# Kernel optimization log

Measured on AMD Instinct MI355X. Metric: run time of the kernel, lower is better.

## Reference

```python
import jax, jax.numpy as jnp
import numpy as np

THRESH = 0.5
DECAY = 0.2

B = 16384
IN_DIM = 784
HID = 400
OUT = 10


def act_fun(mem):
    # spike = (mem > thresh).float()
    return (mem > THRESH).astype(mem.dtype)


def setup_inputs() -> dict:
    key = jax.random.key(0)
    kx, k1, k2, k3, k4 = jax.random.split(key, 5)
    x = jax.random.uniform(kx, (B, IN_DIM), dtype=jnp.float32)  # pixel probs in [0,1]
    W1 = jax.random.normal(k1, (HID, IN_DIM), dtype=jnp.float32) * (1.0 / np.sqrt(IN_DIM))
    b1 = jax.random.normal(k2, (HID,), dtype=jnp.float32) * 0.01
    W2 = jax.random.normal(k3, (OUT, HID), dtype=jnp.float32) * (1.0 / np.sqrt(HID))
    b2 = jax.random.normal(k4, (OUT,), dtype=jnp.float32) * 0.01
    return {"x": x, "W1": W1, "b1": b1, "W2": W2, "b2": b2, "time_window": 20}


def reference(x, W1, b1, W2, b2, time_window):
    Bsz = x.shape[0]
    keys = jax.random.split(jax.random.key(42), time_window)

    def step(carry, k):
        h1_mem, h1_spike, h2_mem, h2_spike, h2_sum = carry
        u = jax.random.uniform(k, x.shape, dtype=x.dtype)
        xi = (x > u).astype(x.dtype)  # Bernoulli spike encoding of input
        # LIF layer 1
        h1_mem = h1_mem * DECAY * (1.0 - h1_spike) + xi @ W1.T + b1
        h1_spike = act_fun(h1_mem)
        # LIF layer 2
        h2_mem = h2_mem * DECAY * (1.0 - h2_spike) + h1_spike @ W2.T + b2
        h2_spike = act_fun(h2_mem)
        return (h1_mem, h1_spike, h2_mem, h2_spike, h2_sum + h2_spike), None

    z_h = jnp.zeros((Bsz, HID), dtype=x.dtype)
    z_o = jnp.zeros((Bsz, OUT), dtype=x.dtype)
    init = (z_h, z_h, z_o, z_o, z_o)
    (_, _, _, _, h2_sum), _ = jax.lax.scan(step, init, keys)
    return h2_sum / time_window
```

## Files before the change

### kernel.cpp

```cpp
#include <hip/hip_runtime.h>
#include <stdint.h>


#define INDIM  784
#define HID    400
#define ODIM   10
#define TSTEPS 20
#define NS     16384

#define KW     25
#define NCOL   416
#define NB_N   13
#define BROWG  202
#define BROWL  203
#define MS     256
#define NLIMB  5

#define XI_DW   ((size_t)TSTEPS * NS * KW)
#define SPK_OFF (XI_DW)
#define SPK_DW  ((size_t)NS * TSTEPS * NB_N)
#define BL_OFF  (XI_DW + SPK_DW)
#define WS_NEED ((XI_DW + SPK_DW + (size_t)NLIMB * NCOL * BROWG) * 4)

#define TD   8
#define NT   98
#define WTJ  512
#define XIW  26
#define SPW  14

typedef int i32x4  __attribute__((ext_vector_type(4)));
typedef int i32x16 __attribute__((ext_vector_type(16)));

__device__ __forceinline__ void tfr(uint32_t& x0, uint32_t& x1, int r) {
  x0 += x1;
  x1 = (x1 << r) | (x1 >> (32 - r));
  x1 ^= x0;
}

__device__ __forceinline__ uint2 tf2x32(uint32_t k0, uint32_t k1,
                                        uint32_t c0, uint32_t c1) {
  uint32_t k2 = k0 ^ k1 ^ 0x1BD11BDAu;
  uint32_t x0 = c0 + k0, x1 = c1 + k1;
  tfr(x0,x1,13); tfr(x0,x1,15); tfr(x0,x1,26); tfr(x0,x1,6);
  x0 += k1; x1 += k2 + 1u;
  tfr(x0,x1,17); tfr(x0,x1,29); tfr(x0,x1,16); tfr(x0,x1,24);
  x0 += k2; x1 += k0 + 2u;
  tfr(x0,x1,13); tfr(x0,x1,15); tfr(x0,x1,26); tfr(x0,x1,6);
  x0 += k0; x1 += k1 + 3u;
  tfr(x0,x1,17); tfr(x0,x1,29); tfr(x0,x1,16); tfr(x0,x1,24);
  x0 += k1; x1 += k2 + 4u;
  tfr(x0,x1,13); tfr(x0,x1,15); tfr(x0,x1,26); tfr(x0,x1,6);
  x0 += k2; x1 += k0 + 5u;
  return make_uint2(x0, x1);
}

__device__ __forceinline__ float bits_to_unif(uint32_t b) {
  return __uint_as_float((b >> 9) | 0x3f800000u) - 1.0f;
}


__global__ __launch_bounds__(256, 4)
void snn_prep(const float* __restrict__ x, const float* __restrict__ W1,
              uint32_t* __restrict__ ws) {
  const int tid = threadIdx.x, bid = blockIdx.x;
  if (bid < 4096) {
    const int wv = tid >> 6, lane = tid & 63;
    const int s  = bid * 4 + wv;
    float xv[13];
#pragma unroll
    for (int c = 0; c < 13; ++c) {
      const int d = c * 64 + lane;
      xv[c] = (d < INDIM) ? x[s * INDIM + d] : 0.0f;
    }
    for (int t = 0; t < TSTEPS; ++t) {
      const uint2 kt = tf2x32(0u, 42u, 0u, (uint32_t)t);
      uint32_t* dst = ws + ((size_t)t * NS + s) * KW;
#pragma unroll
      for (int c = 0; c < 13; ++c) {
        const int d = c * 64 + lane;
        int xb = 0;
        if (d < INDIM) {
          uint2 r = tf2x32(kt.x, kt.y, 0u, (uint32_t)(s * INDIM + d));
          xb = xv[c] > bits_to_unif(r.x ^ r.y);
        }
        unsigned long long m = __ballot(xb);
        if (lane == 0) {
          dst[2*c] = (uint32_t)m;
          if (2*c + 1 < KW) dst[2*c + 1] = (uint32_t)(m >> 32);
        }
      }
    }
  } else {
    const int idx = (bid - 4096) * 256 + tid;
    if (idx < NCOL * BROWG) {
      const int col = idx / BROWG, grp = idx - col * BROWG;
      uint32_t dw[NLIMB] = {0u, 0u, 0u, 0u, 0u};
#pragma unroll
      for (int b = 0; b < 4; ++b) {
        const int d = grp * 4 + b;
        double w = 0.0;
        if (col < HID && d < INDIM) w = (double)W1[col * INDIM + d];
        long long V = (long long)rint(w * 0x1p41);
        const long long CAP = 547599908735ll;
        if (V >  CAP) V =  CAP;
        if (V < -CAP) V = -CAP;
#pragma unroll
        for (int l = 0; l < NLIMB; ++l) {
          const int r = (int)(((V + 128) & 255) - 128);
          dw[l] |= ((uint32_t)(uint8_t)(int8_t)r) << (8 * b);
          V = (V - r) >> 8;
        }
      }
      uint32_t* bl = ws + BL_OFF;
#pragma unroll
      for (int l = 0; l < NLIMB; ++l)
        bl[((size_t)l * NCOL + col) * BROWG + grp] = dw[l];
    }
  }
}

__global__ __launch_bounds__(256, 2)
void snn_l1(const float* __restrict__ b1, uint32_t* __restrict__ ws) {
  __shared__ uint32_t xi_lds[MS * KW];
  __shared__ uint32_t blds[2][32 * BROWL];

  const int tid  = threadIdx.x;
  const int nb   = blockIdx.x % NB_N;
  const int mb   = blockIdx.x / NB_N;
  const int n0   = nb * 32, sbase = mb * MS;
  const int wv   = tid >> 6, lane = tid & 63;
  const int half = lane >> 5, c31 = lane & 31;
  const int col  = n0 + c31;
  const double bb = (col < HID) ? (double)b1[col] : 0.0;

  const uint32_t* xi_ws  = ws;
  uint32_t*       spk_ws = ws + SPK_OFF;
  const uint32_t* bl_ws  = ws + BL_OFF;

  auto stageB = [&](int l, int buf) {
    if (tid < BROWG) {
      const uint32_t* src = bl_ws + ((size_t)l * NCOL + n0) * BROWG + tid;
      uint32_t* dst = &blds[buf][tid];
#pragma unroll
      for (int c = 0; c < 32; ++c)
        dst[c * BROWL] = src[c * BROWG];
    }
  };
  auto stageXi = [&](int t) {
    const uint32_t* src = xi_ws + ((size_t)t * NS + sbase) * KW;
#pragma unroll
    for (int j = 0; j < KW; ++j)
      xi_lds[tid + j * 256] = src[tid + j * 256];
  };

  double mem[2][16];
  uint32_t sp[2] = {0u, 0u};
#pragma unroll
  for (int T = 0; T < 2; ++T)
#pragma unroll
    for (int i = 0; i < 16; ++i) mem[T][i] = 0.0;

  stageB(0, 0);
  stageXi(0);
  __syncthreads();

  int cur = 0;
  for (int t = 0; t < TSTEPS; ++t) {
#pragma unroll
    for (int T = 0; T < 2; ++T)
#pragma unroll
      for (int i = 0; i < 16; ++i)
        mem[T][i] = ((sp[T] >> i) & 1u) ? 0.0 : mem[T][i] * 0.2;

    double sc = 0x1p-41;
    for (int l = 0; l < NLIMB; ++l) {
      stageB((l + 1) % NLIMB, cur ^ 1);

      i32x16 acc0, acc1;
#pragma unroll
      for (int i = 0; i < 16; ++i) { acc0[i] = 0; acc1[i] = 0; }

      const uint32_t* xr0 = &xi_lds[(wv * 64 +  0 + c31) * KW];
      const uint32_t* xr1 = &xi_lds[(wv * 64 + 32 + c31) * KW];
      const uint32_t* bp0 = &blds[cur][c31 * BROWL + half * 4];

#pragma unroll 5
      for (int ks = 0; ks < 25; ++ks) {
        const uint32_t hw0 = (xr0[ks] >> (16 * half)) & 0xFFFFu;
        const uint32_t hw1 = (xr1[ks] >> (16 * half)) & 0xFFFFu;
        i32x4 a0, a1, bfr;
#pragma unroll
        for (int q = 0; q < 4; ++q) {
          a0[q] = (int)((((hw0 >> (4*q)) & 0xFu) * 0x00204081u) & 0x01010101u);
          a1[q] = (int)((((hw1 >> (4*q)) & 0xFu) * 0x00204081u) & 0x01010101u);
        }
        const uint32_t* bp = bp0 + ks * 8;
        const uint2 p0 = *(const uint2*)(bp);
        const uint2 p1 = *(const uint2*)(bp + 2);
        bfr[0] = (int)p0.x; bfr[1] = (int)p0.y;
        bfr[2] = (int)p1.x; bfr[3] = (int)p1.y;
        acc0 = __builtin_amdgcn_mfma_i32_32x32x32_i8(a0, bfr, acc0, 0, 0, 0);
        acc1 = __builtin_amdgcn_mfma_i32_32x32x32_i8(a1, bfr, acc1, 0, 0, 0);
      }

#pragma unroll
      for (int i = 0; i < 16; ++i) {
        mem[0][i] += (double)acc0[i] * sc;
        mem[1][i] += (double)acc1[i] * sc;
      }
      sc *= 256.0;
      __syncthreads();
      cur ^= 1;
    }

    uint32_t m0 = 0u, m1 = 0u;
#pragma unroll
    for (int i = 0; i < 16; ++i) {
      mem[0][i] += bb;  if (mem[0][i] > 0.5) m0 |= (1u << i);
      mem[1][i] += bb;  if (mem[1][i] > 0.5) m1 |= (1u << i);
    }
    sp[0] = m0; sp[1] = m1;

#pragma unroll
    for (int T = 0; T < 2; ++T) {
      const uint32_t mm = T ? m1 : m0;
#pragma unroll
      for (int rg = 0; rg < 16; ++rg) {
        unsigned long long bm = __ballot((mm >> rg) & 1u);
        if (lane == 0) {
          const int rlo  = (rg & 3) + 8 * (rg >> 2);
          const int srow = sbase + wv * 64 + T * 32 + rlo;
          spk_ws[((size_t)srow * TSTEPS + t) * NB_N + nb] = (uint32_t)bm;
          spk_ws[((size_t)(srow + 4) * TSTEPS + t) * NB_N + nb] =
              (uint32_t)(bm >> 32);
        }
      }
    }

    if (t + 1 < TSTEPS) stageXi(t + 1);
    __syncthreads();
  }
}

__global__ __launch_bounds__(256, 4)
void snn_l2(const float* __restrict__ W2, const float* __restrict__ b2,
            const uint32_t* __restrict__ ws, float* __restrict__ out) {
  const int gid    = blockIdx.x * 256 + threadIdx.x;
  const int sample = gid / ODIM;
  const int oc     = gid - sample * ODIM;
  const uint32_t* spk_ws = ws + SPK_OFF;

  double m2 = 0.0; int s2 = 0, cnt2 = 0;
  const double b2r = (double)b2[oc];
  const float4* w2p = (const float4*)(W2 + oc * HID);

  for (int t = 0; t < TSTEPS; ++t) {
    const uint32_t* sw = spk_ws + ((size_t)sample * TSTEPS + t) * NB_N;
    const double a2 = s2 ? 0.0 : m2 * 0.2;
    double d0 = 0.0, d1 = 0.0, d2 = 0.0, d3 = 0.0;
#pragma unroll 2
    for (int w = 0; w < 12; ++w) {
      const uint32_t word = sw[w];
#pragma unroll
      for (int q = 0; q < 8; ++q) {
        const float4 v4 = w2p[8 * w + q];
        const uint32_t nib = (word >> (4 * q)) & 0xFu;
        d0 = fma((double)v4.x, (double)(nib & 1u),        d0);
        d1 = fma((double)v4.y, (double)((nib >> 1) & 1u), d1);
        d2 = fma((double)v4.z, (double)((nib >> 2) & 1u), d2);
        d3 = fma((double)v4.w, (double)((nib >> 3) & 1u), d3);
      }
    }
    {
      const uint32_t word = sw[12] & 0xFFFFu;
#pragma unroll
      for (int q = 0; q < 4; ++q) {
        const float4 v4 = w2p[96 + q];
        const uint32_t nib = (word >> (4 * q)) & 0xFu;
        d0 = fma((double)v4.x, (double)(nib & 1u),        d0);
        d1 = fma((double)v4.y, (double)((nib >> 1) & 1u), d1);
        d2 = fma((double)v4.z, (double)((nib >> 2) & 1u), d2);
        d3 = fma((double)v4.w, (double)((nib >> 3) & 1u), d3);
      }
    }
    m2 = (a2 + ((d0 + d1) + (d2 + d3))) + b2r;
    s2 = (m2 > 0.5) ? 1 : 0;
    cnt2 += s2;
  }
  out[sample * ODIM + oc] = (float)((double)cnt2 / 20.0);
}

__global__ __launch_bounds__(512, 4)
void snn_fused_v6(const float* __restrict__ x,  const float* __restrict__ W1,
                  const float* __restrict__ b1, const float* __restrict__ W2,
                  const float* __restrict__ b2, float* __restrict__ out) {
  __shared__ double   wt[2][TD * WTJ];
  __shared__ uint32_t xib[2][16][XIW];
  __shared__ uint32_t spk[2][16][SPW];

  const int tid  = threadIdx.x;
  const int g    = blockIdx.x;
  const int wv   = tid >> 6;
  const int sg   = wv >> 1;
  const int kh   = wv & 1;
  const int lane = tid & 63;
  const int jb   = 256 * kh + lane;

  for (int i = tid; i < 2 * TD * WTJ; i += 512)
    if ((i & (WTJ - 1)) >= HID) (&wt[0][0])[i] = 0.0;

  double bb[4];
#pragma unroll
  for (int k = 0; k < 4; ++k) {
    const int j = jb + 64 * k;
    bb[k] = (j < HID) ? (double)b1[j] : 0.0;
  }

  double   mem1[4][4];
  double   acc1[4][4];
  uint32_t spv[4];
#pragma unroll
  for (int s = 0; s < 4; ++s) {
    spv[s] = 0u;
#pragma unroll
    for (int k = 0; k < 4; ++k) { mem1[s][k] = 0.0; acc1[s][k] = 0.0; }
  }

  const int ls = tid / ODIM;
  const int lo = tid - ls * ODIM;
  double m2 = 0.0;
  int    s2 = 0, cnt2 = 0;
  const double b2r = (tid < 160) ? (double)b2[lo] : 0.0;

  auto layer2_step = [&](int tt) {
    if (tid < 160) {
      double a2 = s2 ? 0.0 : m2 * 0.2;
      double d0 = 0.0, d1 = 0.0, d2 = 0.0, d3 = 0.0;
      const float4* w2p = (const float4*)(W2 + lo * HID);
#pragma unroll 4
      for (int qq = 0; qq < 100; ++qq) {
        const uint32_t nib = (spk[tt][ls][qq >> 3] >> ((qq & 7) * 4)) & 0xFu;
        const float4 v4 = w2p[qq];
        d0 = fma((double)v4.x, (double)(nib & 1u),        d0);
        d1 = fma((double)v4.y, (double)((nib >> 1) & 1u), d1);
        d2 = fma((double)v4.z, (double)((nib >> 2) & 1u), d2);
        d3 = fma((double)v4.w, (double)((nib >> 3) & 1u), d3);
      }
      m2 = (a2 + ((d0 + d1) + (d2 + d3))) + b2r;
      s2 = (m2 > 0.5) ? 1 : 0;
      cnt2 += s2;
    }
  };

  const bool stager = (tid < HID);
  float4 va = make_float4(0,0,0,0), vb = va;
  if (stager) {
    const float4* s0 = (const float4*)(W1 + tid * INDIM);
    va = s0[0]; vb = s0[1];
    double* dst = &wt[0][tid];
    dst[0*WTJ] = (double)va.x;  dst[1*WTJ] = (double)va.y;
    dst[2*WTJ] = (double)va.z;  dst[3*WTJ] = (double)va.w;
    dst[4*WTJ] = (double)vb.x;  dst[5*WTJ] = (double)vb.y;
    dst[6*WTJ] = (double)vb.z;  dst[7*WTJ] = (double)vb.w;
    const float4* s1 = (const float4*)(W1 + tid * INDIM + TD);
    va = s1[0]; vb = s1[1];
  }
  int cur = 0;
  int ld  = 2;
  __syncthreads();

  for (int tp = 0; tp < TSTEPS / 2; ++tp) {
    const uint2 ka = tf2x32(0u, 42u, 0u, (uint32_t)(2 * tp));
    const uint2 kb = tf2x32(0u, 42u, 0u, (uint32_t)(2 * tp + 1));
    const uint32_t kx[2] = { ka.x, kb.x };
    const uint32_t ky[2] = { ka.y, kb.y };

    const int cA = kh ? 7 : 0;
    const int cB = kh ? 13 : 7;
    for (int s = 0; s < 4; ++s) {
      const int q   = 4 * sg + s;
      const int row = g * 8 + (q & 7) + ((q >= 8) ? 8192 : 0);
      for (int c = cA; c < cB; ++c) {
        const int d = c * 64 + lane;
        const bool valid = (d < INDIM);
        float xv = 0.0f;
        if (valid) xv = x[row * INDIM + d];
        const uint32_t e = (uint32_t)row * (uint32_t)INDIM + (uint32_t)d;
#pragma unroll
        for (int tt = 0; tt < 2; ++tt) {
          int xb = 0;
          if (valid) {
            uint2 r = tf2x32(kx[tt], ky[tt], 0u, e);
            xb = xv > bits_to_unif(r.x ^ r.y);
          }
          unsigned long long m = __ballot(xb);
          if (lane == 0) {
            xib[tt][q][2*c]     = (uint32_t)m;
            xib[tt][q][2*c + 1] = (uint32_t)(m >> 32);
          }
        }
      }
    }
    __syncthreads();

#pragma unroll
    for (int s = 0; s < 4; ++s)
#pragma unroll
      for (int k = 0; k < 4; ++k) {
        mem1[s][k] = ((spv[s] >> k) & 1u) ? 0.0 : mem1[s][k] * 0.2;
        acc1[s][k] = 0.0;
      }

    for (int td = 0; td < NT; ++td) {
      if (stager) {
        double* dst = &wt[cur ^ 1][tid];
        dst[0*WTJ] = (double)va.x;  dst[1*WTJ] = (double)va.y;
        dst[2*WTJ] = (double)va.z;  dst[3*WTJ] = (double)va.w;
        dst[4*WTJ] = (double)vb.x;  dst[5*WTJ] = (double)vb.y;
        dst[6*WTJ] = (double)vb.z;  dst[7*WTJ] = (double)vb.w;
        const float4* src = (const float4*)(W1 + tid * INDIM + ld * TD);
        va = src[0]; vb = src[1];
      }
      ld = (ld + 1 == NT) ? 0 : ld + 1;

      const int wi = td >> 2, sh = (td & 3) * 8;
      uint32_t bA[4], bB[4];
#pragma unroll
      for (int s = 0; s < 4; ++s) {
        bA[s] = (uint32_t)__builtin_amdgcn_readfirstlane(
                  (int)((xib[0][4*sg + s][wi] >> sh) & 0xFFu));
        bB[s] = (uint32_t)__builtin_amdgcn_readfirstlane(
                  (int)((xib[1][4*sg + s][wi] >> sh) & 0xFFu));
      }

      const double* wp = &wt[cur][jb];
#pragma unroll
      for (int dt = 0; dt < TD; ++dt) {
        double wd[4];
#pragma unroll
        for (int k = 0; k < 4; ++k)
          wd[k] = wp[dt * WTJ + 64 * k];
#pragma unroll
        for (int s = 0; s < 4; ++s) {
          if (bA[s] & (1u << dt)) {
#pragma unroll
            for (int k = 0; k < 4; ++k) mem1[s][k] += wd[k];
          }
          if (bB[s] & (1u << dt)) {
#pragma unroll
            for (int k = 0; k < 4; ++k) acc1[s][k] += wd[k];
          }
        }
      }

      __syncthreads();
      cur ^= 1;
    }

#pragma unroll
    for (int s = 0; s < 4; ++s) {
      uint32_t m = 0u;
#pragma unroll
      for (int k = 0; k < 4; ++k) {
        mem1[s][k] += bb[k];
        if (mem1[s][k] > 0.5) m |= (1u << k);
      }
      spv[s] = m;
#pragma unroll
      for (int k = 0; k < 4; ++k) {
        unsigned long long bm = __ballot((m >> k) & 1u);
        const int w0 = 8 * kh + 2 * k;
        if (lane == 0 && w0 < SPW) {
          spk[0][4*sg + s][w0]     = (uint32_t)bm;
          spk[0][4*sg + s][w0 + 1] = (uint32_t)(bm >> 32);
        }
      }
    }

#pragma unroll
    for (int s = 0; s < 4; ++s) {
      uint32_t m = 0u;
#pragma unroll
      for (int k = 0; k < 4; ++k) {
        double v = ((spv[s] >> k) & 1u) ? 0.0 : mem1[s][k] * 0.2;
        v += acc1[s][k];
        v += bb[k];
        mem1[s][k] = v;
        if (v > 0.5) m |= (1u << k);
      }
      spv[s] = m;
#pragma unroll
      for (int k = 0; k < 4; ++k) {
        unsigned long long bm = __ballot((m >> k) & 1u);
        const int w0 = 8 * kh + 2 * k;
        if (lane == 0 && w0 < SPW) {
          spk[1][4*sg + s][w0]     = (uint32_t)bm;
          spk[1][4*sg + s][w0 + 1] = (uint32_t)(bm >> 32);
        }
      }
    }
    __syncthreads();

    layer2_step(0);
    layer2_step(1);
  }

  if (tid < 160) {
    const int row = g * 8 + (ls & 7) + ((ls >= 8) ? 8192 : 0);
    out[row * ODIM + lo] = (float)((double)cnt2 / 20.0);
  }
}

extern "C" void kernel_launch(void* const* d_in, const int* in_sizes, int n_in,
                              void* d_out, int out_size, void* d_ws, size_t ws_size,
                              hipStream_t stream) {
  const float* x  = (const float*)d_in[0];
  const float* W1 = (const float*)d_in[1];
  const float* b1 = (const float*)d_in[2];
  const float* W2 = (const float*)d_in[3];
  const float* b2 = (const float*)d_in[4];
  float* out = (float*)d_out;

  if (d_ws != nullptr && ws_size >= WS_NEED) {
    uint32_t* ws = (uint32_t*)d_ws;
    hipLaunchKernelGGL(snn_prep, dim3(4096 + 329), dim3(256), 0, stream,
                       x, W1, ws);
    hipLaunchKernelGGL(snn_l1, dim3(NB_N * 64), dim3(256), 0, stream, b1, ws);
    hipLaunchKernelGGL(snn_l2, dim3(640), dim3(256), 0, stream, W2, b2, ws, out);
  } else {
    hipLaunchKernelGGL(snn_fused_v6, dim3(1024), dim3(512), 0, stream,
                       x, W1, b1, W2, b2, out);
  }
}
```

Measured before the change: 3.991 ms.

## Keep all W1 limbs resident in LDS and prefetch next xi into registers

The layer-1 kernel now loads all five W1 byte-limbs into shared memory once, instead of re-staging one limb per inner iteration. It computes all limbs' MFMAs in a single k-loop, which drops the per-limb barriers and repeated global reloads. The next timestep's xi tile is prefetched into registers, and the block index is remapped so neighbouring blocks share column tiles. Spike output goes to a transposed layout through an LDS buffer so global writes are coalesced, and layer 2 reads the new layout. The cost is more LDS and register use, including ten accumulator tiles, with occupancy lowered to one block per SIMD group.

```diff
diff --git a/kernel.cpp b/kernel.cpp
--- a/kernel.cpp
+++ b/kernel.cpp
@@ -119,39 +119,49 @@
   }
 }
 
-__global__ __launch_bounds__(256, 2)
+__global__ __launch_bounds__(256, 1)
 void snn_l1(const float* __restrict__ b1, uint32_t* __restrict__ ws) {
+  __shared__ uint32_t blds[NLIMB][32 * BROWL];
   __shared__ uint32_t xi_lds[MS * KW];
-  __shared__ uint32_t blds[2][32 * BROWL];
-
-  const int tid  = threadIdx.x;
-  const int nb   = blockIdx.x % NB_N;
-  const int mb   = blockIdx.x / NB_N;
-  const int n0   = nb * 32, sbase = mb * MS;
-  const int wv   = tid >> 6, lane = tid & 63;
+  __shared__ uint32_t spkbuf[MS];
+
+  const int tid = threadIdx.x;
+  const int bid = blockIdx.x;
+  const int x8  = bid & 7;
+  const int q   = bid >> 3;
+  const int nb  = q % NB_N;
+  const int mb  = x8 + 8 * (q / NB_N);
+  const int n0  = nb * 32, sbase = mb * MS;
+  const int wv  = tid >> 6, lane = tid & 63;
   const int half = lane >> 5, c31 = lane & 31;
-  const int col  = n0 + c31;
+  const int col = n0 + c31;
   const double bb = (col < HID) ? (double)b1[col] : 0.0;
 
   const uint32_t* xi_ws  = ws;
   uint32_t*       spk_ws = ws + SPK_OFF;
   const uint32_t* bl_ws  = ws + BL_OFF;
 
-  auto stageB = [&](int l, int buf) {
-    if (tid < BROWG) {
-      const uint32_t* src = bl_ws + ((size_t)l * NCOL + n0) * BROWG + tid;
-      uint32_t* dst = &blds[buf][tid];
-#pragma unroll
-      for (int c = 0; c < 32; ++c)
-        dst[c * BROWL] = src[c * BROWG];
-    }
-  };
-  auto stageXi = [&](int t) {
-    const uint32_t* src = xi_ws + ((size_t)t * NS + sbase) * KW;
+  for (int i = tid; i < NLIMB * 32 * BROWG; i += 256) {
+    const int l  = i / (32 * BROWG);
+    const int r  = i - l * (32 * BROWG);
+    const int c  = r / BROWG;
+    const int gd = r - c * BROWG;
+    blds[l][c * BROWL + gd] =
+        bl_ws[((size_t)l * NCOL + n0 + c) * BROWG + gd];
+  }
+  {
+    const uint32_t* src = xi_ws + ((size_t)0 * NS + sbase) * KW;
 #pragma unroll
     for (int j = 0; j < KW; ++j)
       xi_lds[tid + j * 256] = src[tid + j * 256];
-  };
+  }
+  uint32_t pf[KW];
+  {
+    const uint32_t* src = xi_ws + ((size_t)1 * NS + sbase) * KW;
+#pragma unroll
+    for (int j = 0; j < KW; ++j) pf[j] = src[tid + j * 256];
+  }
+  __syncthreads();
 
   double mem[2][16];
   uint32_t sp[2] = {0u, 0u};
@@ -160,11 +170,10 @@
 #pragma unroll
     for (int i = 0; i < 16; ++i) mem[T][i] = 0.0;
 
-  stageB(0, 0);
-  stageXi(0);
-  __syncthreads();
-
-  int cur = 0;
+  const uint32_t* xr0 = &xi_lds[(wv * 64 +  0 + c31) * KW];
+  const uint32_t* xr1 = &xi_lds[(wv * 64 + 32 + c31) * KW];
+  const uint32_t* bb0 = &blds[0][c31 * BROWL + half * 4];
+
   for (int t = 0; t < TSTEPS; ++t) {
 #pragma unroll
     for (int T = 0; T < 2; ++T)
@@ -172,45 +181,48 @@
       for (int i = 0; i < 16; ++i)
         mem[T][i] = ((sp[T] >> i) & 1u) ? 0.0 : mem[T][i] * 0.2;
 
-    double sc = 0x1p-41;
-    for (int l = 0; l < NLIMB; ++l) {
-      stageB((l + 1) % NLIMB, cur ^ 1);
-
-      i32x16 acc0, acc1;
-#pragma unroll
-      for (int i = 0; i < 16; ++i) { acc0[i] = 0; acc1[i] = 0; }
-
-      const uint32_t* xr0 = &xi_lds[(wv * 64 +  0 + c31) * KW];
-      const uint32_t* xr1 = &xi_lds[(wv * 64 + 32 + c31) * KW];
-      const uint32_t* bp0 = &blds[cur][c31 * BROWL + half * 4];
+    i32x16 acc[NLIMB][2];
+#pragma unroll
+    for (int l = 0; l < NLIMB; ++l)
+#pragma unroll
+      for (int T = 0; T < 2; ++T)
+#pragma unroll
+        for (int i = 0; i < 16; ++i) acc[l][T][i] = 0;
 
 #pragma unroll 5
-      for (int ks = 0; ks < 25; ++ks) {
-        const uint32_t hw0 = (xr0[ks] >> (16 * half)) & 0xFFFFu;
-        const uint32_t hw1 = (xr1[ks] >> (16 * half)) & 0xFFFFu;
-        i32x4 a0, a1, bfr;
-#pragma unroll
-        for (int q = 0; q < 4; ++q) {
-          a0[q] = (int)((((hw0 >> (4*q)) & 0xFu) * 0x00204081u) & 0x01010101u);
-          a1[q] = (int)((((hw1 >> (4*q)) & 0xFu) * 0x00204081u) & 0x01010101u);
-        }
-        const uint32_t* bp = bp0 + ks * 8;
+    for (int ks = 0; ks < 25; ++ks) {
+      const uint32_t hw0 = (xr0[ks] >> (16 * half)) & 0xFFFFu;
+      const uint32_t hw1 = (xr1[ks] >> (16 * half)) & 0xFFFFu;
+      i32x4 a0, a1;
+#pragma unroll
+      for (int qq = 0; qq < 4; ++qq) {
+        a0[qq] = (int)((((hw0 >> (4*qq)) & 0xFu) * 0x00204081u) & 0x01010101u);
+        a1[qq] = (int)((((hw1 >> (4*qq)) & 0xFu) * 0x00204081u) & 0x01010101u);
+      }
+#pragma unroll
+      for (int l = 0; l < NLIMB; ++l) {
+        const uint32_t* bp = bb0 + l * (32 * BROWL) + ks * 8;
         const uint2 p0 = *(const uint2*)(bp);
         const uint2 p1 = *(const uint2*)(bp + 2);
+        i32x4 bfr;
         bfr[0] = (int)p0.x; bfr[1] = (int)p0.y;
         bfr[2] = (int)p1.x; bfr[3] = (int)p1.y;
-        acc0 = __builtin_amdgcn_mfma_i32_32x32x32_i8(a0, bfr, acc0, 0, 0, 0);
-        acc1 = __builtin_amdgcn_mfma_i32_32x32x32_i8(a1, bfr, acc1, 0, 0, 0);
-      }
-
+        acc[l][0] = __builtin_amdgcn_mfma_i32_32x32x32_i8(a0, bfr, acc[l][0],
+                                                          0, 0, 0);
+        acc[l][1] = __builtin_amdgcn_mfma_i32_32x32x32_i8(a1, bfr, acc[l][1],
+                                                          0, 0, 0);
+      }
+    }
+
+    double sc = 0x1p-41;
+#pragma unroll
+    for (int l = 0; l < NLIMB; ++l) {
 #pragma unroll
       for (int i = 0; i < 16; ++i) {
-        mem[0][i] += (double)acc0[i] * sc;
-        mem[1][i] += (double)acc1[i] * sc;
+        mem[0][i] += (double)acc[l][0][i] * sc;
+        mem[1][i] += (double)acc[l][1][i] * sc;
       }
       sc *= 256.0;
-      __syncthreads();
-      cur ^= 1;
     }
 
     uint32_t m0 = 0u, m1 = 0u;
@@ -228,17 +240,26 @@
       for (int rg = 0; rg < 16; ++rg) {
         unsigned long long bm = __ballot((mm >> rg) & 1u);
         if (lane == 0) {
-          const int rlo  = (rg & 3) + 8 * (rg >> 2);
-          const int srow = sbase + wv * 64 + T * 32 + rlo;
-          spk_ws[((size_t)srow * TSTEPS + t) * NB_N + nb] = (uint32_t)bm;
-          spk_ws[((size_t)(srow + 4) * TSTEPS + t) * NB_N + nb] =
-              (uint32_t)(bm >> 32);
-        }
-      }
-    }
-
-    if (t + 1 < TSTEPS) stageXi(t + 1);
+          const int rlo = (rg & 3) + 8 * (rg >> 2);
+          const int sl  = wv * 64 + T * 32 + rlo;
+          spkbuf[sl]     = (uint32_t)bm;
+          spkbuf[sl + 4] = (uint32_t)(bm >> 32);
+        }
+      }
+    }
     __syncthreads();
+
+    spk_ws[((size_t)nb * TSTEPS + t) * NS + sbase + tid] = spkbuf[tid];
+
+    if (t + 1 < TSTEPS) {
+#pragma unroll
+      for (int j = 0; j < KW; ++j) xi_lds[tid + j * 256] = pf[j];
+      const int tn = (t + 2 < TSTEPS) ? t + 2 : TSTEPS - 1;
+      const uint32_t* src = xi_ws + ((size_t)tn * NS + sbase) * KW;
+#pragma unroll
+      for (int j = 0; j < KW; ++j) pf[j] = src[tid + j * 256];
+      __syncthreads();
+    }
   }
 }
 
@@ -255,16 +276,21 @@
   const float4* w2p = (const float4*)(W2 + oc * HID);
 
   for (int t = 0; t < TSTEPS; ++t) {
-    const uint32_t* sw = spk_ws + ((size_t)sample * TSTEPS + t) * NB_N;
+    uint32_t sw[NB_N];
+#pragma unroll
+    for (int w = 0; w < NB_N; ++w)
+      sw[w] = spk_ws[((size_t)w * TSTEPS + t) * NS + sample];
+    sw[12] &= 0xFFFFu;
+
     const double a2 = s2 ? 0.0 : m2 * 0.2;
     double d0 = 0.0, d1 = 0.0, d2 = 0.0, d3 = 0.0;
 #pragma unroll 2
     for (int w = 0; w < 12; ++w) {
       const uint32_t word = sw[w];
 #pragma unroll
-      for (int q = 0; q < 8; ++q) {
-        const float4 v4 = w2p[8 * w + q];
-        const uint32_t nib = (word >> (4 * q)) & 0xFu;
+      for (int qq = 0; qq < 8; ++qq) {
+        const float4 v4 = w2p[8 * w + qq];
+        const uint32_t nib = (word >> (4 * qq)) & 0xFu;
         d0 = fma((double)v4.x, (double)(nib & 1u),        d0);
         d1 = fma((double)v4.y, (double)((nib >> 1) & 1u), d1);
         d2 = fma((double)v4.z, (double)((nib >> 2) & 1u), d2);
@@ -272,11 +298,11 @@
       }
     }
     {
-      const uint32_t word = sw[12] & 0xFFFFu;
-#pragma unroll
-      for (int q = 0; q < 4; ++q) {
-        const float4 v4 = w2p[96 + q];
-        const uint32_t nib = (word >> (4 * q)) & 0xFu;
+      const uint32_t word = sw[12];
+#pragma unroll
+      for (int qq = 0; qq < 4; ++qq) {
+        const float4 v4 = w2p[96 + qq];
+        const uint32_t nib = (word >> (4 * qq)) & 0xFu;
         d0 = fma((double)v4.x, (double)(nib & 1u),        d0);
         d1 = fma((double)v4.y, (double)((nib >> 1) & 1u), d1);
         d2 = fma((double)v4.z, (double)((nib >> 2) & 1u), d2);
@@ -525,7 +551,8 @@
     uint32_t* ws = (uint32_t*)d_ws;
     hipLaunchKernelGGL(snn_prep, dim3(4096 + 329), dim3(256), 0, stream,
                        x, W1, ws);
-    hipLaunchKernelGGL(snn_l1, dim3(NB_N * 64), dim3(256), 0, stream, b1, ws);
+    hipLaunchKernelGGL(snn_l1, dim3(8 * NB_N * 8), dim3(256), 0, stream,
+                       b1, ws);
     hipLaunchKernelGGL(snn_l2, dim3(640), dim3(256), 0, stream, W2, b2, ws, out);
   } else {
     hipLaunchKernelGGL(snn_fused_v6, dim3(1024), dim3(512), 0, stream,
```

Result: faster. 3.477 ms (-12.9%).
